# Kernel optimization log

Measured on AMD Instinct MI355X. Metric: run time of the kernel, lower is better.

Reference implementation:

```python
import jax, jax.numpy as jnp
import numpy as np

B, H, W = 128, 48, 48
CEN_IN, CEN_OUT, DIR_IN, DIR_OUT, CEN_K, DIR_K = 32, 32, 24, 24, 3, 5
C_IN = CEN_IN + 4 * DIR_IN  # central + 4 directional groups (hor, ver, diag, anti-diag)


def _dwconv(x, k):
    # x: [B, C, H, W], k: [C, kh, kw] depthwise kernels -> SAME-padded depthwise conv
    C = x.shape[1]
    return jax.lax.conv_general_dilated(
        x, k[:, None], window_strides=(1, 1), padding='SAME',
        dimension_numbers=('NCHW', 'OIHW', 'NCHW'), feature_group_count=C)


def setup_inputs() -> dict:
    key = jax.random.key(0)
    ks = jax.random.split(key, 8)
    s = 0.1
    return {
        'x': jax.random.normal(ks[0], (B, C_IN, H, W), dtype=jnp.float32),
        'cen_tensor': jax.random.normal(ks[1], (CEN_IN, CEN_K, CEN_K), dtype=jnp.float32) * s,
        'dir_tensor': jax.random.normal(ks[2], (DIR_IN, DIR_K), dtype=jnp.float32) * s,
        'cen2cen': jax.random.normal(ks[3], (CEN_OUT, CEN_IN), dtype=jnp.float32) * s,
        'par2cen': jax.random.normal(ks[4], (CEN_OUT, DIR_IN), dtype=jnp.float32) * s,
        'dia2cen': jax.random.normal(ks[5], (CEN_OUT, DIR_IN), dtype=jnp.float32) * s,
        'cen2dir': jax.random.normal(ks[6], (DIR_OUT, CEN_IN), dtype=jnp.float32) * s,
        'dir2dir': jax.random.normal(ks[7], (DIR_OUT, DIR_IN), dtype=jnp.float32) * s,
    }


def reference(x, cen_tensor, dir_tensor, cen2cen, par2cen, dia2cen, cen2dir, dir2dir):
    cen_in = cen_tensor.shape[0]
    dir_in, K = dir_tensor.shape
    # split channel groups: [cen | hor | ver | diag | anti-diag]
    xc = x[:, :cen_in]
    xh = x[:, cen_in:cen_in + dir_in]
    xv = x[:, cen_in + dir_in:cen_in + 2 * dir_in]
    xd1 = x[:, cen_in + 2 * dir_in:cen_in + 3 * dir_in]
    xd2 = x[:, cen_in + 3 * dir_in:]
    eye = jnp.eye(K, dtype=x.dtype)
    # --- directional depthwise stage ---
    yc = _dwconv(xc, cen_tensor)                                # full 2D kernel per channel
    yh = _dwconv(xh, dir_tensor[:, None, :])
    yv = _dwconv(xv, dir_tensor[:, :, None])                    # K x 1 vertical line
    yd1 = _dwconv(xd1, dir_tensor[:, :, None] * eye)            # main diagonal line
    yd2 = _dwconv(xd2, dir_tensor[:, :, None] * eye[:, ::-1])   # anti-diagonal line
    # --- directional pointwise (1x1) mixing stage ---
    mix = lambda Wm, t: jnp.einsum('oc,bchw->bohw', Wm, t)
    out_cen = mix(cen2cen, yc) + mix(par2cen, yh + yv) + mix(dia2cen, yd1 + yd2)
    od_cen = mix(cen2dir, yc)
    out_dirs = [od_cen + mix(dir2dir, t) for t in (yh, yv, yd1, yd2)]
    return jnp.concatenate([out_cen] + out_dirs, axis=1)
```

## Files before the change

### kernel.cpp

```cpp
#include <hip/hip_runtime.h>
#include <hip/hip_bf16.h>


namespace {
constexpr int HH = 48, WW = 48, HW = HH * WW;
constexpr int C_IN = 128, C_OUT = 128, NB = 128;
constexpr int RPB = 8;
constexpr int NSTR = HH / RPB;
constexpr int PIX = RPB * WW;
constexpr int NT = 512;
constexpr int CHK = 16;
constexpr int NCHK = C_IN / CHK;
constexpr int XR = RPB + 4;
constexpr int QR = 17;
constexpr int XROWF = QR * 4;
constexpr int XQ = CHK * XR * QR;
constexpr int YCS = 392;
constexpr int NBLK = NB * NSTR;
constexpr size_t M_BYTES = 128 * 128 * 2;
constexpr size_t ZB_OFF = M_BYTES;
}

typedef __attribute__((ext_vector_type(8))) short bf16x8;
typedef __attribute__((ext_vector_type(4))) float f32x4;

__device__ __forceinline__ ushort f2bf(float f) {
    __hip_bfloat16 h = __float2bfloat16(f);
    return *reinterpret_cast<ushort*>(&h);
}

__global__ void build_M(const float* __restrict__ c2c, const float* __restrict__ p2c,
                        const float* __restrict__ d2c, const float* __restrict__ c2d,
                        const float* __restrict__ d2dW, ushort* __restrict__ Mbf) {
    int t = blockIdx.x * 256 + threadIdx.x;
    if (t >= 128 * 128) return;
    int o = t & 127, c = t >> 7;
    float v;
    if (o < 32) {
        if (c < 32)       v = c2c[o * 32 + c];
        else if (c < 56)  v = p2c[o * 24 + c - 32];
        else if (c < 80)  v = p2c[o * 24 + c - 56];
        else if (c < 104) v = d2c[o * 24 + c - 80];
        else              v = d2c[o * 24 + c - 104];
    } else {
        int g = (o - 32) / 24, oo = (o - 32) % 24;
        if (c < 32) v = c2d[oo * 32 + c];
        else {
            int gc = (c - 32) / 24, cc2 = (c - 32) % 24;
            v = (gc == g) ? d2dW[oo * 24 + cc2] : 0.f;
        }
    }
    Mbf[o * 128 + c] = f2bf(v);
}

__global__ __launch_bounds__(NT) void dsc_fused(
    const float* __restrict__ x,
    const float* __restrict__ cen_t,
    const float* __restrict__ dir_t,
    const ushort* __restrict__ Mbf,
    const float* __restrict__ zb,
    float* __restrict__ out)
{
    __shared__ float  xs[XQ * 4];
    __shared__ ushort yT[PIX * 128];
    __shared__ ushort ycp[CHK * YCS];

    const int tid = threadIdx.x;
    const int bid = (blockIdx.x & 7) * (NBLK / 8) + (blockIdx.x >> 3);
    const int b   = bid / NSTR;
    const int h0  = (bid % NSTR) * RPB;
    const float* __restrict__ xb = x + (size_t)b * C_IN * HW;

    auto stage = [&](int t) {
        const int c0 = t * CHK;
#pragma unroll
        for (int k = 0; k < 7; ++k) {
            int d = tid + k * NT;
            if (d < XQ) {
                int q  = d % QR;
                int cr = d / QR;
                int r  = cr % XR;
                int c  = cr / XR;
                int gh = h0 - 2 + r;
                bool ok = ((unsigned)gh < (unsigned)HH) && (q < 12);
                const float* src = ok ? (xb + (size_t)(c0 + c) * HW + gh * WW + q * 4) : zb;
                __builtin_amdgcn_global_load_lds(
                    (const __attribute__((address_space(1))) unsigned int*)src,
                    (__attribute__((address_space(3))) unsigned int*)(xs + (size_t)d * 4),
                    16, 0, 0);
            }
        }
    };

    auto dwconv = [&](int t) {
        const int c0 = t * CHK;
#pragma unroll
        for (int k = 0; k < 2; ++k) {
            int task = tid + k * NT;
            if (task >= CHK * 48) break;
            int c   = task / 48;
            int pg  = task % 48;
            int row = pg & 7;
            int w0  = (pg >> 3) * 8;
            int cc  = c0 + c;
            const float* xr0 = xs + (size_t)(c * XR) * XROWF;
            float acv[8];
#pragma unroll
            for (int j = 0; j < 8; ++j) acv[j] = 0.f;

            if (cc < 32) {
#pragma unroll
                for (int i = 0; i < 3; ++i) {
                    const float* xr = xr0 + (row + 1 + i) * XROWF;
                    float4 A = *(const float4*)&xr[(w0 - 4) & 63];
                    float4 B = *(const float4*)&xr[w0];
                    float4 C = *(const float4*)&xr[w0 + 4];
                    float4 D = *(const float4*)&xr[(w0 + 8) & 63];
                    float win[16] = {A.x,A.y,A.z,A.w, B.x,B.y,B.z,B.w,
                                     C.x,C.y,C.z,C.w, D.x,D.y,D.z,D.w};
                    float k0 = cen_t[cc*9 + i*3 + 0];
                    float k1 = cen_t[cc*9 + i*3 + 1];
                    float k2 = cen_t[cc*9 + i*3 + 2];
#pragma unroll
                    for (int j = 0; j < 8; ++j)
                        acv[j] += k0*win[j+3] + k1*win[j+4] + k2*win[j+5];
                }
            } else if (cc < 56) {
                int cd = cc - 32;
                const float* xr = xr0 + (row + 2) * XROWF;
                float4 A = *(const float4*)&xr[(w0 - 4) & 63];
                float4 B = *(const float4*)&xr[w0];
                float4 C = *(const float4*)&xr[w0 + 4];
                float4 D = *(const float4*)&xr[(w0 + 8) & 63];
                float win[16] = {A.x,A.y,A.z,A.w, B.x,B.y,B.z,B.w,
                                 C.x,C.y,C.z,C.w, D.x,D.y,D.z,D.w};
#pragma unroll
                for (int i = 0; i < 5; ++i) {
                    float tt = dir_t[cd*5 + i];
#pragma unroll
                    for (int j = 0; j < 8; ++j) acv[j] += tt * win[j+2+i];
                }
            } else if (cc < 80) {
                int cd = cc - 56;
#pragma unroll
                for (int i = 0; i < 5; ++i) {
                    const float* xr = xr0 + (row + i) * XROWF;
                    float4 B = *(const float4*)&xr[w0];
                    float4 C = *(const float4*)&xr[w0 + 4];
                    float w8[8] = {B.x,B.y,B.z,B.w, C.x,C.y,C.z,C.w};
                    float tt = dir_t[cd*5 + i];
#pragma unroll
                    for (int j = 0; j < 8; ++j) acv[j] += tt * w8[j];
                }
            } else {
                int cd  = (cc < 104) ? cc - 80 : cc - 104;
                bool d1 = (cc < 104);
#pragma unroll
                for (int i = 0; i < 5; ++i) {
                    const float* xr = xr0 + (row + i) * XROWF;
                    float4 A = *(const float4*)&xr[(w0 - 4) & 63];
                    float4 B = *(const float4*)&xr[w0];
                    float4 C = *(const float4*)&xr[w0 + 4];
                    float4 D = *(const float4*)&xr[(w0 + 8) & 63];
                    float win[16] = {A.x,A.y,A.z,A.w, B.x,B.y,B.z,B.w,
                                     C.x,C.y,C.z,C.w, D.x,D.y,D.z,D.w};
                    float tt = dir_t[cd*5 + i];
                    if (d1) {
#pragma unroll
                        for (int j = 0; j < 8; ++j) acv[j] += tt * win[j+2+i];
                    } else {
#pragma unroll
                        for (int j = 0; j < 8; ++j) acv[j] += tt * win[j+6-i];
                    }
                }
            }

            union { ushort us[8]; uint4 v4; } s;
#pragma unroll
            for (int j = 0; j < 8; ++j) s.us[j] = f2bf(acv[j]);
            *(uint4*)&ycp[c * YCS + row * 48 + w0] = s.v4;
        }
    };

    auto transpose = [&](int t) {
#pragma unroll
        for (int k = 0; k < 2; ++k) {
            int task = tid + k * NT;
            if (task >= 2 * PIX) break;
            int gg = task / PIX;
            int p  = task % PIX;
            int g  = t * 2 + gg;
            union { ushort us[8]; uint4 v4; } s;
#pragma unroll
            for (int j = 0; j < 8; ++j) s.us[j] = ycp[(gg * 8 + j) * YCS + p];
            int byte = p * 256 + ((g ^ (p & 7)) << 4);
            *(uint4*)((char*)yT + byte) = s.v4;
        }
    };

    stage(0);
    __syncthreads();
    for (int t = 0; t < NCHK; ++t) {
        dwconv(t);
        __syncthreads();
        if (t + 1 < NCHK) stage(t + 1);
        transpose(t);
        __syncthreads();
    }

    const int l     = tid & 63;
    const int wv    = tid >> 6;
    const int ofr   = wv & 3;
    const int phalf = wv >> 2;
    float* __restrict__ ob = out + (size_t)b * C_OUT * HW + h0 * WW;

    bf16x8 afr[2][4];
#pragma unroll
    for (int pass = 0; pass < 2; ++pass)
#pragma unroll
        for (int kb = 0; kb < 4; ++kb) {
            int o0 = pass * 64 + ofr * 16;
            afr[pass][kb] = *(const bf16x8*)(Mbf + (o0 + (l & 15)) * 128 + kb * 32 + (l >> 4) * 8);
        }

    f32x4 acc[2][12] = {};
#pragma unroll
    for (int kb = 0; kb < 4; ++kb) {
        int g = kb * 4 + (l >> 4);
#pragma unroll
        for (int pf = 0; pf < 12; ++pf) {
            int p = (phalf * 12 + pf) * 16 + (l & 15);
            const bf16x8 bfr = *(const bf16x8*)((const char*)yT + p * 256 + ((g ^ (p & 7)) << 4));
            acc[0][pf] = __builtin_amdgcn_mfma_f32_16x16x32_bf16(afr[0][kb], bfr, acc[0][pf], 0, 0, 0);
            acc[1][pf] = __builtin_amdgcn_mfma_f32_16x16x32_bf16(afr[1][kb], bfr, acc[1][pf], 0, 0, 0);
        }
    }

#pragma unroll
    for (int pass = 0; pass < 2; ++pass) {
        int o0 = pass * 64 + ofr * 16;
#pragma unroll
        for (int pf = 0; pf < 12; ++pf) {
            int p = (phalf * 12 + pf) * 16 + (l & 15);
            int obase = o0 + (l >> 4) * 4;
#pragma unroll
            for (int r = 0; r < 4; ++r)
                ob[(size_t)(obase + r) * HW + p] = acc[pass][pf][r];
        }
    }
}

extern "C" void kernel_launch(void* const* d_in, const int* in_sizes, int n_in,
                              void* d_out, int out_size, void* d_ws, size_t ws_size,
                              hipStream_t stream) {
    const float* x     = (const float*)d_in[0];
    const float* cen_t = (const float*)d_in[1];
    const float* dir_t = (const float*)d_in[2];
    const float* c2c   = (const float*)d_in[3];
    const float* p2c   = (const float*)d_in[4];
    const float* d2c   = (const float*)d_in[5];
    const float* c2d   = (const float*)d_in[6];
    const float* d2dW  = (const float*)d_in[7];
    float* out = (float*)d_out;

    ushort* Mbf = (ushort*)d_ws;
    float*  zb  = (float*)((char*)d_ws + ZB_OFF);

    hipMemsetAsync(zb, 0, 64, stream);
    build_M<<<64, 256, 0, stream>>>(c2c, p2c, d2c, c2d, d2dW, Mbf);
    dsc_fused<<<NBLK, NT, 0, stream>>>(x, cen_t, dir_t, Mbf, zb, out);
}
```

Baseline: 96.47 us.

## Double-buffer input staging and write dwconv results directly into transposed layout

Halves the channel chunk to 8 and double-buffers the LDS input tile, so the async global-to-LDS load of the next chunk is issued before the current chunk's depthwise convolution, leaving one barrier per iteration instead of two. The intermediate ycp buffer and the separate transpose pass are removed: each thread now writes its bf16 results as scattered 2-byte stores straight into the swizzled yT layout. The aim is to overlap load latency with compute and drop a sync and an LDS round trip. In exchange there are twice as many iterations, only 384 of 512 threads do dwconv work, and the narrow scattered LDS stores may cause bank conflicts.

```diff
diff --git a/kernel.cpp b/kernel.cpp
--- a/kernel.cpp
+++ b/kernel.cpp
@@ -9,13 +9,12 @@
 constexpr int NSTR = HH / RPB;
 constexpr int PIX = RPB * WW;
 constexpr int NT = 512;
-constexpr int CHK = 16;
+constexpr int CHK = 8;
 constexpr int NCHK = C_IN / CHK;
 constexpr int XR = RPB + 4;
 constexpr int QR = 17;
 constexpr int XROWF = QR * 4;
 constexpr int XQ = CHK * XR * QR;
-constexpr int YCS = 392;
 constexpr int NBLK = NB * NSTR;
 constexpr size_t M_BYTES = 128 * 128 * 2;
 constexpr size_t ZB_OFF = M_BYTES;
@@ -61,9 +60,8 @@
     const float* __restrict__ zb,
     float* __restrict__ out)
 {
-    __shared__ float  xs[XQ * 4];
+    __shared__ float  xs[2][XQ * 4];
     __shared__ ushort yT[PIX * 128];
-    __shared__ ushort ycp[CHK * YCS];
 
     const int tid = threadIdx.x;
     const int bid = (blockIdx.x & 7) * (NBLK / 8) + (blockIdx.x >> 3);
@@ -71,10 +69,10 @@
     const int h0  = (bid % NSTR) * RPB;
     const float* __restrict__ xb = x + (size_t)b * C_IN * HW;
 
-    auto stage = [&](int t) {
+    auto stage = [&](int t, int buf) {
         const int c0 = t * CHK;
 #pragma unroll
-        for (int k = 0; k < 7; ++k) {
+        for (int k = 0; k < 4; ++k) {
             int d = tid + k * NT;
             if (d < XQ) {
                 int q  = d % QR;
@@ -86,24 +84,20 @@
                 const float* src = ok ? (xb + (size_t)(c0 + c) * HW + gh * WW + q * 4) : zb;
                 __builtin_amdgcn_global_load_lds(
                     (const __attribute__((address_space(1))) unsigned int*)src,
-                    (__attribute__((address_space(3))) unsigned int*)(xs + (size_t)d * 4),
+                    (__attribute__((address_space(3))) unsigned int*)(&xs[buf][0] + (size_t)d * 4),
                     16, 0, 0);
             }
         }
     };
 
-    auto dwconv = [&](int t) {
-        const int c0 = t * CHK;
-#pragma unroll
-        for (int k = 0; k < 2; ++k) {
-            int task = tid + k * NT;
-            if (task >= CHK * 48) break;
-            int c   = task / 48;
-            int pg  = task % 48;
+    auto dwconv = [&](int t, int buf) {
+        if (tid < CHK * 48) {
+            int c   = tid & 7;
+            int pg  = tid >> 3;
             int row = pg & 7;
             int w0  = (pg >> 3) * 8;
-            int cc  = c0 + c;
-            const float* xr0 = xs + (size_t)(c * XR) * XROWF;
+            int cc  = t * CHK + c;
+            const float* xr0 = &xs[buf][0] + (size_t)(c * XR) * XROWF;
             float acv[8];
 #pragma unroll
             for (int j = 0; j < 8; ++j) acv[j] = 0.f;
@@ -175,36 +169,21 @@
                 }
             }
 
-            union { ushort us[8]; uint4 v4; } s;
-#pragma unroll
-            for (int j = 0; j < 8; ++j) s.us[j] = f2bf(acv[j]);
-            *(uint4*)&ycp[c * YCS + row * 48 + w0] = s.v4;
+#pragma unroll
+            for (int j = 0; j < 8; ++j) {
+                int jj = (j + row) & 7;
+                int p  = row * 48 + w0 + jj;
+                int byte = p * 256 + ((t ^ jj) << 4) + c * 2;
+                *(ushort*)((char*)yT + byte) = f2bf(acv[jj]);
+            }
         }
     };
 
-    auto transpose = [&](int t) {
-#pragma unroll
-        for (int k = 0; k < 2; ++k) {
-            int task = tid + k * NT;
-            if (task >= 2 * PIX) break;
-            int gg = task / PIX;
-            int p  = task % PIX;
-            int g  = t * 2 + gg;
-            union { ushort us[8]; uint4 v4; } s;
-#pragma unroll
-            for (int j = 0; j < 8; ++j) s.us[j] = ycp[(gg * 8 + j) * YCS + p];
-            int byte = p * 256 + ((g ^ (p & 7)) << 4);
-            *(uint4*)((char*)yT + byte) = s.v4;
-        }
-    };
-
-    stage(0);
+    stage(0, 0);
     __syncthreads();
     for (int t = 0; t < NCHK; ++t) {
-        dwconv(t);
-        __syncthreads();
-        if (t + 1 < NCHK) stage(t + 1);
-        transpose(t);
+        if (t + 1 < NCHK) stage(t + 1, (t + 1) & 1);
+        dwconv(t, t & 1);
         __syncthreads();
     }
 
```

Result: slower. 129.9 us (+34.7%).
